# Performance work log

Measured on AMD Instinct MI355X. Metric: run time of the kernel, lower is better.

The kernel has to match this reference:

```python
import jax, jax.numpy as jnp
import numpy as np
import math

EMBED_DIM = 1024
WINDOW = 512


def setup_inputs() -> dict:
    key = jax.random.key(0)
    k_x, k_mb, k_wg, k_bg = jax.random.split(key, 4)
    x = jax.random.normal(k_x, (4, 4096, EMBED_DIM), dtype=jnp.float32)
    memory_bank = jax.random.normal(k_mb, (WINDOW, EMBED_DIM), dtype=jnp.float32)
    # memory_gate: nn.Linear(embed_dim, embed_dim)
    lim = 1.0 / math.sqrt(EMBED_DIM)
    gate_w = jax.random.uniform(k_wg, (EMBED_DIM, EMBED_DIM), jnp.float32, -lim, lim)
    gate_b = jax.random.uniform(k_bg, (EMBED_DIM,), jnp.float32, -lim, lim)
    return {"x": x, "memory_bank": memory_bank, "gate_w": gate_w, "gate_b": gate_b}


def reference(x, memory_bank, gate_w, gate_b):
    d = x.shape[-1]
    # attention scores over fixed memory bank: [B, S, W]
    scores = jnp.einsum("bsd,wd->bsw", x, memory_bank) / jnp.sqrt(jnp.asarray(d, x.dtype))
    attn = jax.nn.softmax(scores, axis=-1)
    retrieved = jnp.einsum("bsw,wd->bsd", attn, memory_bank)
    gate = jax.nn.sigmoid(jnp.einsum("bsd,ed->bse", x, gate_w) + gate_b)
    return gate * x + (1.0 - gate) * retrieved
```

## Files before the change

kernel.cpp:

```cpp
#include <hip/hip_runtime.h>
#include <hip/hip_bf16.h>

#define EMBED 1024
#define WINDOW 512
#define NROWS 16384

typedef __attribute__((ext_vector_type(4))) float f32x4;
typedef __bf16 bf16x8 __attribute__((ext_vector_type(8)));

#define GLDS(g, l)                                                        \
  __builtin_amdgcn_global_load_lds(                                       \
      (const __attribute__((address_space(1))) void*)(const void*)(g),    \
      (__attribute__((address_space(3))) void*)(void*)(l), 16, 0, 0)

__global__ __launch_bounds__(256) void cast_bf16_kernel(
    const float* __restrict__ in, __bf16* __restrict__ out, int n8) {
  int i = blockIdx.x * blockDim.x + threadIdx.x;
  if (i >= n8) return;
  const f32x4* p = (const f32x4*)(in + (size_t)i * 8);
  f32x4 a = p[0], b = p[1];
  bf16x8 o = {(__bf16)a[0], (__bf16)a[1], (__bf16)a[2], (__bf16)a[3],
              (__bf16)b[0], (__bf16)b[1], (__bf16)b[2], (__bf16)b[3]};
  *(bf16x8*)(out + (size_t)i * 8) = o;
}

__global__ __launch_bounds__(256) void transpose_mb_kernel(
    const float* __restrict__ mb, __bf16* __restrict__ mbt) {
  int idx = blockIdx.x * blockDim.x + threadIdx.x;
  int w = idx >> 10, d = idx & 1023;
  mbt[(size_t)d * WINDOW + w] = (__bf16)mb[idx];
}

__global__ __launch_bounds__(256) void softmax_kernel(__bf16* __restrict__ s1) {
  const int row = blockIdx.x * 4 + (threadIdx.x >> 6);
  const int lane = threadIdx.x & 63;
  __bf16* p = s1 + (size_t)row * WINDOW + lane * 8;
  bf16x8 v = *(const bf16x8*)p;
  float f[8];
  float mx = -1e30f;
#pragma unroll
  for (int j = 0; j < 8; ++j) {
    f[j] = (float)v[j] * 0.03125f;
    mx = fmaxf(mx, f[j]);
  }
#pragma unroll
  for (int off = 1; off < 64; off <<= 1) mx = fmaxf(mx, __shfl_xor(mx, off));
  float s = 0.f;
#pragma unroll
  for (int j = 0; j < 8; ++j) {
    f[j] = __expf(f[j] - mx);
    s += f[j];
  }
#pragma unroll
  for (int off = 1; off < 64; off <<= 1) s += __shfl_xor(s, off);
  const float inv = 1.0f / s;
  bf16x8 o;
#pragma unroll
  for (int j = 0; j < 8; ++j) o[j] = (__bf16)(f[j] * inv);
  *(bf16x8*)p = o;
}


#define LOADFRAGS(cb, kk)                                                     \
  {                                                                           \
    const __bf16* As_ = &ldsA[cb][(warp_m * 64 + fr) * 64];                   \
    const __bf16* Bs_ = &ldsB[cb][(warp_n * 64 + fr) * 64];                   \
    const int pg_ = (((kk)*4 + fq) ^ (fr & 7)) * 8;                           \
    _Pragma("unroll") for (int m = 0; m < 4; ++m)                             \
        af[m] = *(const bf16x8*)(As_ + m * 16 * 64 + pg_);                    \
    _Pragma("unroll") for (int n = 0; n < 4; ++n)                             \
        bfv[n] = *(const bf16x8*)(Bs_ + n * 16 * 64 + pg_);                   \
  }

#define MFMA16(ACC)                                                           \
  {                                                                           \
    __builtin_amdgcn_s_barrier();                                             \
    asm volatile("s_waitcnt lgkmcnt(0)" ::: "memory");                        \
    __builtin_amdgcn_s_setprio(1);                                            \
    _Pragma("unroll") for (int m = 0; m < 4; ++m)                             \
        _Pragma("unroll") for (int n = 0; n < 4; ++n)                         \
            ACC[m][n] = __builtin_amdgcn_mfma_f32_16x16x32_bf16(              \
                af[m], bfv[n], ACC[m][n], 0, 0, 0);                           \
    __builtin_amdgcn_s_setprio(0);                                            \
    __builtin_amdgcn_s_barrier();                                             \
  }

#define WAIT6 asm volatile("s_waitcnt vmcnt(6)" ::: "memory")
#define WAIT0 asm volatile("s_waitcnt vmcnt(0)" ::: "memory")

__global__ __launch_bounds__(512, 2) void gemm_scores_kernel(
    const __bf16* __restrict__ xb, const __bf16* __restrict__ mbb,
    __bf16* __restrict__ s1) {
  __shared__ __align__(16) __bf16 ldsA[3][256 * 64];
  __shared__ __align__(16) __bf16 ldsB[3][128 * 64];
  const int tid = threadIdx.x;
  const int lane = tid & 63;
  const int wave = tid >> 6;
  const int bid = blockIdx.x;
  const int xcd = bid & 7;
  const int idx = bid >> 3;
  const int bm = xcd * 8 + (idx & 7);
  const int bn = idx >> 3;
  const int row0 = bm * 256;
  const int col0 = bn * 128;
  const int warp_m = wave >> 1;
  const int warp_n = wave & 1;
  const int srow = lane >> 3;
  const int sgc = (lane & 7) ^ srow;
  const int wv32 = wave * 32;
  const int wv16 = wave * 16;
  const int fr = lane & 15;
  const int fq = lane >> 4;

  const __bf16* aS = xb + (size_t)(row0 + wv32 + srow) * EMBED + sgc * 8;
  const __bf16* bS = mbb + (size_t)(col0 + wv16 + srow) * EMBED + sgc * 8;

#define STAGE_S1(vt, buf)                                                     \
  {                                                                           \
    const int k0_ = (vt)*64;                                                  \
    _Pragma("unroll") for (int c = 0; c < 2; ++c)                             \
        GLDS(aS + (size_t)c * 8 * EMBED + k0_, &ldsA[buf][(wv32 + c * 8) * 64]); \
    GLDS(bS + k0_, &ldsB[buf][wv16 * 64]);                                    \
  }
#define STAGE_S2(vt, buf)                                                     \
  {                                                                           \
    const int k0_ = (vt)*64;                                                  \
    _Pragma("unroll") for (int c = 2; c < 4; ++c)                             \
        GLDS(aS + (size_t)c * 8 * EMBED + k0_, &ldsA[buf][(wv32 + c * 8) * 64]); \
    GLDS(bS + (size_t)8 * EMBED + k0_, &ldsB[buf][(wv16 + 8) * 64]);          \
  }

  f32x4 acc[4][4];
#pragma unroll
  for (int m = 0; m < 4; ++m)
#pragma unroll
    for (int n = 0; n < 4; ++n) acc[m][n] = (f32x4){0.f, 0.f, 0.f, 0.f};
  bf16x8 af[4], bfv[4];

  STAGE_S1(0, 0); STAGE_S2(0, 0);
  STAGE_S1(1, 1); STAGE_S2(1, 1);
  WAIT6;
  __builtin_amdgcn_s_barrier();

  const int NT = 16;
  for (int vt = 0; vt < NT; ++vt) {
    const int cb = vt % 3;
    const int nb = (vt + 2) % 3;
    LOADFRAGS(cb, 0);
    if (vt + 2 < NT) STAGE_S1(vt + 2, nb);
    MFMA16(acc);
    LOADFRAGS(cb, 1);
    if (vt + 2 < NT) STAGE_S2(vt + 2, nb);
    if (vt < NT - 2) { WAIT6; } else if (vt == NT - 2) { WAIT0; }
    MFMA16(acc);
  }
#undef STAGE_S1
#undef STAGE_S2

#pragma unroll
  for (int n = 0; n < 4; ++n) {
    const int col = col0 + warp_n * 64 + n * 16 + fr;
#pragma unroll
    for (int m = 0; m < 4; ++m)
#pragma unroll
      for (int j = 0; j < 4; ++j) {
        const int row = row0 + warp_m * 64 + m * 16 + fq * 4 + j;
        s1[(size_t)row * WINDOW + col] = (__bf16)acc[m][n][j];
      }
  }
}

__global__ __launch_bounds__(512, 2) void dual_fused_kernel(
    const __bf16* __restrict__ s1, const __bf16* __restrict__ xb,
    const __bf16* __restrict__ mbt, const __bf16* __restrict__ gwb,
    const float* __restrict__ gb, float* __restrict__ out) {
  __shared__ __align__(16) __bf16 ldsA[3][256 * 64];
  __shared__ __align__(16) __bf16 ldsB[3][128 * 64];
  const int tid = threadIdx.x;
  const int lane = tid & 63;
  const int wave = tid >> 6;
  const int bid = blockIdx.x;
  const int xcd = bid & 7;
  const int idx = bid >> 3;
  const int bm = xcd * 8 + (idx & 7);
  const int bn = idx >> 3;
  const int row0 = bm * 256;
  const int col0 = bn * 128;
  const int warp_m = wave >> 1;
  const int warp_n = wave & 1;
  const int srow = lane >> 3;
  const int sgc = (lane & 7) ^ srow;
  const int wv32 = wave * 32;
  const int wv16 = wave * 16;
  const int fr = lane & 15;
  const int fq = lane >> 4;

  const __bf16* aR = s1 + (size_t)(row0 + wv32 + srow) * WINDOW + sgc * 8;
  const __bf16* bR = mbt + (size_t)(col0 + wv16 + srow) * WINDOW + sgc * 8;
  const __bf16* aG = xb + (size_t)(row0 + wv32 + srow) * EMBED + sgc * 8;
  const __bf16* bG = gwb + (size_t)(col0 + wv16 + srow) * EMBED + sgc * 8;

#define STAGE_D1(vt, buf)                                                     \
  {                                                                           \
    if ((vt) < 8) {                                                           \
      const int k0_ = (vt)*64;                                                \
      _Pragma("unroll") for (int c = 0; c < 2; ++c)                           \
          GLDS(aR + (size_t)c * 8 * WINDOW + k0_,                             \
               &ldsA[buf][(wv32 + c * 8) * 64]);                              \
      GLDS(bR + k0_, &ldsB[buf][wv16 * 64]);                                  \
    } else {                                                                  \
      const int k0_ = ((vt)-8) * 64;                                          \
      _Pragma("unroll") for (int c = 0; c < 2; ++c)                           \
          GLDS(aG + (size_t)c * 8 * EMBED + k0_,                              \
               &ldsA[buf][(wv32 + c * 8) * 64]);                              \
      GLDS(bG + k0_, &ldsB[buf][wv16 * 64]);                                  \
    }                                                                         \
  }
#define STAGE_D2(vt, buf)                                                     \
  {                                                                           \
    if ((vt) < 8) {                                                           \
      const int k0_ = (vt)*64;                                                \
      _Pragma("unroll") for (int c = 2; c < 4; ++c)                           \
          GLDS(aR + (size_t)c * 8 * WINDOW + k0_,                             \
               &ldsA[buf][(wv32 + c * 8) * 64]);                              \
      GLDS(bR + (size_t)8 * WINDOW + k0_, &ldsB[buf][(wv16 + 8) * 64]);       \
    } else {                                                                  \
      const int k0_ = ((vt)-8) * 64;                                          \
      _Pragma("unroll") for (int c = 2; c < 4; ++c)                           \
          GLDS(aG + (size_t)c * 8 * EMBED + k0_,                              \
               &ldsA[buf][(wv32 + c * 8) * 64]);                              \
      GLDS(bG + (size_t)8 * EMBED + k0_, &ldsB[buf][(wv16 + 8) * 64]);        \
    }                                                                         \
  }

  f32x4 accr[4][4], accg[4][4];
#pragma unroll
  for (int m = 0; m < 4; ++m)
#pragma unroll
    for (int n = 0; n < 4; ++n) {
      accr[m][n] = (f32x4){0.f, 0.f, 0.f, 0.f};
      accg[m][n] = (f32x4){0.f, 0.f, 0.f, 0.f};
    }
  bf16x8 af[4], bfv[4];

  STAGE_D1(0, 0); STAGE_D2(0, 0);
  STAGE_D1(1, 1); STAGE_D2(1, 1);
  WAIT6;
  __builtin_amdgcn_s_barrier();

  const int NT = 24;
  for (int vt = 0; vt < 8; ++vt) {
    const int cb = vt % 3;
    const int nb = (vt + 2) % 3;
    LOADFRAGS(cb, 0);
    STAGE_D1(vt + 2, nb);
    MFMA16(accr);
    LOADFRAGS(cb, 1);
    STAGE_D2(vt + 2, nb);
    WAIT6;
    MFMA16(accr);
  }
  for (int vt = 8; vt < NT; ++vt) {
    const int cb = vt % 3;
    const int nb = (vt + 2) % 3;
    LOADFRAGS(cb, 0);
    if (vt + 2 < NT) STAGE_D1(vt + 2, nb);
    MFMA16(accg);
    LOADFRAGS(cb, 1);
    if (vt + 2 < NT) STAGE_D2(vt + 2, nb);
    if (vt < NT - 2) { WAIT6; } else if (vt == NT - 2) { WAIT0; }
    MFMA16(accg);
  }
#undef STAGE_D1
#undef STAGE_D2

#pragma unroll
  for (int n = 0; n < 4; ++n) {
    const int col = col0 + warp_n * 64 + n * 16 + fr;
    const float bias = gb[col];
#pragma unroll
    for (int m = 0; m < 4; ++m) {
#pragma unroll
      for (int j = 0; j < 4; ++j) {
        const int row = row0 + warp_m * 64 + m * 16 + fq * 4 + j;
        const size_t o = (size_t)row * EMBED + col;
        const float g = 1.0f / (1.0f + __expf(-(accg[m][n][j] + bias)));
        const float xv = (float)xb[o];
        out[o] = g * xv + (1.0f - g) * accr[m][n][j];
      }
    }
  }
}

extern "C" void kernel_launch(void* const* d_in, const int* in_sizes, int n_in,
                              void* d_out, int out_size, void* d_ws,
                              size_t ws_size, hipStream_t stream) {
  const float* x = (const float*)d_in[0];
  const float* mb = (const float*)d_in[1];
  const float* gw = (const float*)d_in[2];
  const float* gb = (const float*)d_in[3];
  float* out = (float*)d_out;

  char* ws = (char*)d_ws;
  __bf16* xb = (__bf16*)(ws);
  __bf16* mbb = (__bf16*)(ws + 33554432);
  __bf16* mbt = (__bf16*)(ws + 34603008);
  __bf16* gwb = (__bf16*)(ws + 35651584);
  __bf16* s1 = (__bf16*)(ws + 37748736);

  cast_bf16_kernel<<<8192, 256, 0, stream>>>(x, xb, 2097152);
  cast_bf16_kernel<<<256, 256, 0, stream>>>(mb, mbb, 65536);
  cast_bf16_kernel<<<512, 256, 0, stream>>>(gw, gwb, 131072);
  transpose_mb_kernel<<<2048, 256, 0, stream>>>(mb, mbt);
  gemm_scores_kernel<<<256, 512, 0, stream>>>(xb, mbb, s1);
  softmax_kernel<<<4096, 256, 0, stream>>>(s1);
  dual_fused_kernel<<<512, 512, 0, stream>>>(s1, xb, mbt, gwb, gb, out);
}
```

Before: 125.5 us.

## Split dual fused GEMM into two 256x256-tile GEMMs with intermediate buffer

```diff
diff --git a/kernel.cpp b/kernel.cpp
--- a/kernel.cpp
+++ b/kernel.cpp
@@ -60,8 +60,7 @@
   *(bf16x8*)p = o;
 }
 
-
-#define LOADFRAGS(cb, kk)                                                     \
+#define SLOADFRAGS(cb, kk)                                                    \
   {                                                                           \
     const __bf16* As_ = &ldsA[cb][(warp_m * 64 + fr) * 64];                   \
     const __bf16* Bs_ = &ldsB[cb][(warp_n * 64 + fr) * 64];                   \
@@ -72,7 +71,7 @@
         bfv[n] = *(const bf16x8*)(Bs_ + n * 16 * 64 + pg_);                   \
   }
 
-#define MFMA16(ACC)                                                           \
+#define SMFMA16(ACC)                                                          \
   {                                                                           \
     __builtin_amdgcn_s_barrier();                                             \
     asm volatile("s_waitcnt lgkmcnt(0)" ::: "memory");                        \
@@ -84,9 +83,6 @@
     __builtin_amdgcn_s_setprio(0);                                            \
     __builtin_amdgcn_s_barrier();                                             \
   }
-
-#define WAIT6 asm volatile("s_waitcnt vmcnt(6)" ::: "memory")
-#define WAIT0 asm volatile("s_waitcnt vmcnt(0)" ::: "memory")
 
 __global__ __launch_bounds__(512, 2) void gemm_scores_kernel(
     const __bf16* __restrict__ xb, const __bf16* __restrict__ mbb,
@@ -139,20 +135,24 @@
 
   STAGE_S1(0, 0); STAGE_S2(0, 0);
   STAGE_S1(1, 1); STAGE_S2(1, 1);
-  WAIT6;
+  asm volatile("s_waitcnt vmcnt(6)" ::: "memory");
   __builtin_amdgcn_s_barrier();
 
   const int NT = 16;
   for (int vt = 0; vt < NT; ++vt) {
     const int cb = vt % 3;
     const int nb = (vt + 2) % 3;
-    LOADFRAGS(cb, 0);
+    SLOADFRAGS(cb, 0);
     if (vt + 2 < NT) STAGE_S1(vt + 2, nb);
-    MFMA16(acc);
-    LOADFRAGS(cb, 1);
+    SMFMA16(acc);
+    SLOADFRAGS(cb, 1);
     if (vt + 2 < NT) STAGE_S2(vt + 2, nb);
-    if (vt < NT - 2) { WAIT6; } else if (vt == NT - 2) { WAIT0; }
-    MFMA16(acc);
+    if (vt < NT - 2) {
+      asm volatile("s_waitcnt vmcnt(6)" ::: "memory");
+    } else if (vt == NT - 2) {
+      asm volatile("s_waitcnt vmcnt(0)" ::: "memory");
+    }
+    SMFMA16(acc);
   }
 #undef STAGE_S1
 #undef STAGE_S2
@@ -170,123 +170,117 @@
   }
 }
 
-__global__ __launch_bounds__(512, 2) void dual_fused_kernel(
-    const __bf16* __restrict__ s1, const __bf16* __restrict__ xb,
-    const __bf16* __restrict__ mbt, const __bf16* __restrict__ gwb,
-    const float* __restrict__ gb, float* __restrict__ out) {
-  __shared__ __align__(16) __bf16 ldsA[3][256 * 64];
-  __shared__ __align__(16) __bf16 ldsB[3][128 * 64];
-  const int tid = threadIdx.x;
-  const int lane = tid & 63;
-  const int wave = tid >> 6;
+template <int NT, int LDA_, int LDB_, int EPI>
+__global__ __launch_bounds__(512, 2) void gemm_mt_kernel(
+    const __bf16* __restrict__ A, const __bf16* __restrict__ B,
+    const float* __restrict__ gb, __bf16* __restrict__ rbb,
+    float* __restrict__ out) {
+  __shared__ __align__(16) __bf16 ldsA[4][256 * 32];
+  __shared__ __align__(16) __bf16 ldsB[4][256 * 32];
+  const int tid = threadIdx.x, lane = tid & 63, wave = tid >> 6;
   const int bid = blockIdx.x;
-  const int xcd = bid & 7;
-  const int idx = bid >> 3;
-  const int bm = xcd * 8 + (idx & 7);
-  const int bn = idx >> 3;
-  const int row0 = bm * 256;
-  const int col0 = bn * 128;
-  const int warp_m = wave >> 1;
-  const int warp_n = wave & 1;
-  const int srow = lane >> 3;
-  const int sgc = (lane & 7) ^ srow;
-  const int wv32 = wave * 32;
-  const int wv16 = wave * 16;
-  const int fr = lane & 15;
-  const int fq = lane >> 4;
-
-  const __bf16* aR = s1 + (size_t)(row0 + wv32 + srow) * WINDOW + sgc * 8;
-  const __bf16* bR = mbt + (size_t)(col0 + wv16 + srow) * WINDOW + sgc * 8;
-  const __bf16* aG = xb + (size_t)(row0 + wv32 + srow) * EMBED + sgc * 8;
-  const __bf16* bG = gwb + (size_t)(col0 + wv16 + srow) * EMBED + sgc * 8;
-
-#define STAGE_D1(vt, buf)                                                     \
-  {                                                                           \
-    if ((vt) < 8) {                                                           \
-      const int k0_ = (vt)*64;                                                \
-      _Pragma("unroll") for (int c = 0; c < 2; ++c)                           \
-          GLDS(aR + (size_t)c * 8 * WINDOW + k0_,                             \
-               &ldsA[buf][(wv32 + c * 8) * 64]);                              \
-      GLDS(bR + k0_, &ldsB[buf][wv16 * 64]);                                  \
-    } else {                                                                  \
-      const int k0_ = ((vt)-8) * 64;                                          \
-      _Pragma("unroll") for (int c = 0; c < 2; ++c)                           \
-          GLDS(aG + (size_t)c * 8 * EMBED + k0_,                              \
-               &ldsA[buf][(wv32 + c * 8) * 64]);                              \
-      GLDS(bG + k0_, &ldsB[buf][wv16 * 64]);                                  \
-    }                                                                         \
-  }
-#define STAGE_D2(vt, buf)                                                     \
-  {                                                                           \
-    if ((vt) < 8) {                                                           \
-      const int k0_ = (vt)*64;                                                \
-      _Pragma("unroll") for (int c = 2; c < 4; ++c)                           \
-          GLDS(aR + (size_t)c * 8 * WINDOW + k0_,                             \
-               &ldsA[buf][(wv32 + c * 8) * 64]);                              \
-      GLDS(bR + (size_t)8 * WINDOW + k0_, &ldsB[buf][(wv16 + 8) * 64]);       \
-    } else {                                                                  \
-      const int k0_ = ((vt)-8) * 64;                                          \
-      _Pragma("unroll") for (int c = 2; c < 4; ++c)                           \
-          GLDS(aG + (size_t)c * 8 * EMBED + k0_,                              \
-               &ldsA[buf][(wv32 + c * 8) * 64]);                              \
-      GLDS(bG + (size_t)8 * EMBED + k0_, &ldsB[buf][(wv16 + 8) * 64]);        \
-    }                                                                         \
-  }
-
-  f32x4 accr[4][4], accg[4][4];
-#pragma unroll
-  for (int m = 0; m < 4; ++m)
-#pragma unroll
-    for (int n = 0; n < 4; ++n) {
-      accr[m][n] = (f32x4){0.f, 0.f, 0.f, 0.f};
-      accg[m][n] = (f32x4){0.f, 0.f, 0.f, 0.f};
+  const int bm = (bid & 7) * 8 + ((bid >> 3) & 7);
+  const int bn = bid >> 6;
+  const int row0 = bm * 256, col0 = bn * 256;
+  const int warp_m = wave >> 2;
+  const int warp_n = wave & 3;
+  const int fr = lane & 15, fq = lane >> 4;
+
+  const int lrow = lane >> 2;
+  const int lsg = (lane & 3) ^ ((lane >> 3) & 3);
+  const __bf16* aSrc = A + (size_t)(row0 + wave * 32 + lrow) * LDA_ + lsg * 8;
+  const __bf16* bSrc = B + (size_t)(col0 + wave * 32 + lrow) * LDB_ + lsg * 8;
+
+#define STG_A(t, c)                                                           \
+  GLDS(aSrc + (size_t)(c) * 16 * LDA_ + (t) * 32,                             \
+       &ldsA[(t) & 3][(wave * 32 + (c) * 16) * 32])
+#define STG_B(t, c)                                                           \
+  GLDS(bSrc + (size_t)(c) * 16 * LDB_ + (t) * 32,                             \
+       &ldsB[(t) & 3][(wave * 32 + (c) * 16) * 32])
+
+  f32x4 acc[8][4];
+#pragma unroll
+  for (int m = 0; m < 8; ++m)
+#pragma unroll
+    for (int n = 0; n < 4; ++n) acc[m][n] = (f32x4){0.f, 0.f, 0.f, 0.f};
+  bf16x8 af[4], bfv[4];
+  const int gA = (fq ^ ((fr >> 1) & 3)) * 8;
+
+  STG_A(0, 0); STG_A(0, 1); STG_B(0, 0); STG_B(0, 1);
+  STG_A(1, 0); STG_A(1, 1); STG_B(1, 0); STG_B(1, 1);
+  STG_A(2, 0); STG_A(2, 1); STG_B(2, 0); STG_B(2, 1);
+  asm volatile("s_waitcnt vmcnt(8)" ::: "memory");
+  __builtin_amdgcn_s_barrier();
+
+  for (int t = 0; t < NT; ++t) {
+    const int s = t & 3;
+    const __bf16* As = &ldsA[s][(warp_m * 128 + fr) * 32 + gA];
+    const __bf16* Bs = &ldsB[s][(warp_n * 64 + fr) * 32 + gA];
+#pragma unroll
+    for (int m = 0; m < 4; ++m) af[m] = *(const bf16x8*)(As + m * 16 * 32);
+#pragma unroll
+    for (int n = 0; n < 4; ++n) bfv[n] = *(const bf16x8*)(Bs + n * 16 * 32);
+    if (t + 3 < NT) { STG_A(t + 3, 0); STG_A(t + 3, 1); }
+    __builtin_amdgcn_s_barrier();
+    asm volatile("s_waitcnt lgkmcnt(0)" ::: "memory");
+    __builtin_amdgcn_s_setprio(1);
+#pragma unroll
+    for (int m = 0; m < 4; ++m)
+#pragma unroll
+      for (int n = 0; n < 4; ++n)
+        acc[m][n] = __builtin_amdgcn_mfma_f32_16x16x32_bf16(af[m], bfv[n],
+                                                            acc[m][n], 0, 0, 0);
+    __builtin_amdgcn_s_setprio(0);
+    __builtin_amdgcn_s_barrier();
+#pragma unroll
+    for (int m = 0; m < 4; ++m)
+      af[m] = *(const bf16x8*)(As + (64 + m * 16) * 32);
+    if (t + 3 < NT) { STG_B(t + 3, 0); STG_B(t + 3, 1); }
+    if (t + 1 < NT) {
+      if (t + 3 < NT) {
+        asm volatile("s_waitcnt vmcnt(8)" ::: "memory");
+      } else if (t + 2 < NT) {
+        asm volatile("s_waitcnt vmcnt(4)" ::: "memory");
+      } else {
+        asm volatile("s_waitcnt vmcnt(0)" ::: "memory");
+      }
     }
-  bf16x8 af[4], bfv[4];
-
-  STAGE_D1(0, 0); STAGE_D2(0, 0);
-  STAGE_D1(1, 1); STAGE_D2(1, 1);
-  WAIT6;
-  __builtin_amdgcn_s_barrier();
-
-  const int NT = 24;
-  for (int vt = 0; vt < 8; ++vt) {
-    const int cb = vt % 3;
-    const int nb = (vt + 2) % 3;
-    LOADFRAGS(cb, 0);
-    STAGE_D1(vt + 2, nb);
-    MFMA16(accr);
-    LOADFRAGS(cb, 1);
-    STAGE_D2(vt + 2, nb);
-    WAIT6;
-    MFMA16(accr);
-  }
-  for (int vt = 8; vt < NT; ++vt) {
-    const int cb = vt % 3;
-    const int nb = (vt + 2) % 3;
-    LOADFRAGS(cb, 0);
-    if (vt + 2 < NT) STAGE_D1(vt + 2, nb);
-    MFMA16(accg);
-    LOADFRAGS(cb, 1);
-    if (vt + 2 < NT) STAGE_D2(vt + 2, nb);
-    if (vt < NT - 2) { WAIT6; } else if (vt == NT - 2) { WAIT0; }
-    MFMA16(accg);
-  }
-#undef STAGE_D1
-#undef STAGE_D2
+    __builtin_amdgcn_s_barrier();
+    asm volatile("s_waitcnt lgkmcnt(0)" ::: "memory");
+    __builtin_amdgcn_s_setprio(1);
+#pragma unroll
+    for (int m = 0; m < 4; ++m)
+#pragma unroll
+      for (int n = 0; n < 4; ++n)
+        acc[4 + m][n] = __builtin_amdgcn_mfma_f32_16x16x32_bf16(
+            af[m], bfv[n], acc[4 + m][n], 0, 0, 0);
+    __builtin_amdgcn_s_setprio(0);
+    __builtin_amdgcn_s_barrier();
+  }
+#undef STG_A
+#undef STG_B
 
 #pragma unroll
   for (int n = 0; n < 4; ++n) {
     const int col = col0 + warp_n * 64 + n * 16 + fr;
-    const float bias = gb[col];
-#pragma unroll
-    for (int m = 0; m < 4; ++m) {
+    float bias = 0.f;
+    if (EPI == 1 || EPI == 3) bias = gb[col];
+#pragma unroll
+    for (int m = 0; m < 8; ++m) {
 #pragma unroll
       for (int j = 0; j < 4; ++j) {
-        const int row = row0 + warp_m * 64 + m * 16 + fq * 4 + j;
+        const int row = row0 + warp_m * 128 + m * 16 + fq * 4 + j;
         const size_t o = (size_t)row * EMBED + col;
-        const float g = 1.0f / (1.0f + __expf(-(accg[m][n][j] + bias)));
-        const float xv = (float)xb[o];
-        out[o] = g * xv + (1.0f - g) * accr[m][n][j];
+        if (EPI == 0) {
+          rbb[o] = (__bf16)acc[m][n][j];
+        } else if (EPI == 2) {
+          out[o] = acc[m][n][j];
+        } else {
+          const float g = 1.0f / (1.0f + __expf(-(acc[m][n][j] + bias)));
+          const float xv = (float)A[(size_t)row * EMBED + col];
+          const float rv = (EPI == 1) ? (float)rbb[o] : out[o];
+          out[o] = g * xv + (1.0f - g) * rv;
+        }
       }
     }
   }
@@ -307,6 +301,8 @@
   __bf16* mbt = (__bf16*)(ws + 34603008);
   __bf16* gwb = (__bf16*)(ws + 35651584);
   __bf16* s1 = (__bf16*)(ws + 37748736);
+  __bf16* rbb = (__bf16*)(ws + 54525952);
+  const bool ws_big = ws_size >= 88080384ull;
 
   cast_bf16_kernel<<<8192, 256, 0, stream>>>(x, xb, 2097152);
   cast_bf16_kernel<<<256, 256, 0, stream>>>(mb, mbb, 65536);
@@ -314,5 +310,15 @@
   transpose_mb_kernel<<<2048, 256, 0, stream>>>(mb, mbt);
   gemm_scores_kernel<<<256, 512, 0, stream>>>(xb, mbb, s1);
   softmax_kernel<<<4096, 256, 0, stream>>>(s1);
-  dual_fused_kernel<<<512, 512, 0, stream>>>(s1, xb, mbt, gwb, gb, out);
-}
+  if (ws_big) {
+    gemm_mt_kernel<16, WINDOW, WINDOW, 0><<<256, 512, 0, stream>>>(
+        s1, mbt, gb, rbb, out);
+    gemm_mt_kernel<32, EMBED, EMBED, 1><<<256, 512, 0, stream>>>(
+        xb, gwb, gb, rbb, out);
+  } else {
+    gemm_mt_kernel<16, WINDOW, WINDOW, 2><<<256, 512, 0, stream>>>(
+        s1, mbt, gb, nullptr, out);
+    gemm_mt_kernel<32, EMBED, EMBED, 3><<<256, 512, 0, stream>>>(
+        xb, gwb, gb, nullptr, out);
+  }
+}
```

New measurement: 159.5 us. 1.27x slower.

## Shrink dual fused GEMM to 128x128 tiles with double-buffered staging

Applied to the files above, without the earlier changes.

```diff
diff --git a/kernel.cpp b/kernel.cpp
--- a/kernel.cpp
+++ b/kernel.cpp
@@ -60,8 +60,7 @@
   *(bf16x8*)p = o;
 }
 
-
-#define LOADFRAGS(cb, kk)                                                     \
+#define SLOADFRAGS(cb, kk)                                                    \
   {                                                                           \
     const __bf16* As_ = &ldsA[cb][(warp_m * 64 + fr) * 64];                   \
     const __bf16* Bs_ = &ldsB[cb][(warp_n * 64 + fr) * 64];                   \
@@ -72,7 +71,7 @@
         bfv[n] = *(const bf16x8*)(Bs_ + n * 16 * 64 + pg_);                   \
   }
 
-#define MFMA16(ACC)                                                           \
+#define SMFMA16(ACC)                                                          \
   {                                                                           \
     __builtin_amdgcn_s_barrier();                                             \
     asm volatile("s_waitcnt lgkmcnt(0)" ::: "memory");                        \
@@ -84,9 +83,6 @@
     __builtin_amdgcn_s_setprio(0);                                            \
     __builtin_amdgcn_s_barrier();                                             \
   }
-
-#define WAIT6 asm volatile("s_waitcnt vmcnt(6)" ::: "memory")
-#define WAIT0 asm volatile("s_waitcnt vmcnt(0)" ::: "memory")
 
 __global__ __launch_bounds__(512, 2) void gemm_scores_kernel(
     const __bf16* __restrict__ xb, const __bf16* __restrict__ mbb,
@@ -139,20 +135,24 @@
 
   STAGE_S1(0, 0); STAGE_S2(0, 0);
   STAGE_S1(1, 1); STAGE_S2(1, 1);
-  WAIT6;
+  asm volatile("s_waitcnt vmcnt(6)" ::: "memory");
   __builtin_amdgcn_s_barrier();
 
   const int NT = 16;
   for (int vt = 0; vt < NT; ++vt) {
     const int cb = vt % 3;
     const int nb = (vt + 2) % 3;
-    LOADFRAGS(cb, 0);
+    SLOADFRAGS(cb, 0);
     if (vt + 2 < NT) STAGE_S1(vt + 2, nb);
-    MFMA16(acc);
-    LOADFRAGS(cb, 1);
+    SMFMA16(acc);
+    SLOADFRAGS(cb, 1);
     if (vt + 2 < NT) STAGE_S2(vt + 2, nb);
-    if (vt < NT - 2) { WAIT6; } else if (vt == NT - 2) { WAIT0; }
-    MFMA16(acc);
+    if (vt < NT - 2) {
+      asm volatile("s_waitcnt vmcnt(6)" ::: "memory");
+    } else if (vt == NT - 2) {
+      asm volatile("s_waitcnt vmcnt(0)" ::: "memory");
+    }
+    SMFMA16(acc);
   }
 #undef STAGE_S1
 #undef STAGE_S2
@@ -170,66 +170,75 @@
   }
 }
 
-__global__ __launch_bounds__(512, 2) void dual_fused_kernel(
+__global__ __launch_bounds__(256, 2) void dual_fused128_kernel(
     const __bf16* __restrict__ s1, const __bf16* __restrict__ xb,
     const __bf16* __restrict__ mbt, const __bf16* __restrict__ gwb,
     const float* __restrict__ gb, float* __restrict__ out) {
-  __shared__ __align__(16) __bf16 ldsA[3][256 * 64];
-  __shared__ __align__(16) __bf16 ldsB[3][128 * 64];
-  const int tid = threadIdx.x;
-  const int lane = tid & 63;
-  const int wave = tid >> 6;
+  __shared__ __align__(16) __bf16 ldsA[2][128 * 64];
+  __shared__ __align__(16) __bf16 ldsB[2][128 * 64];
+  const int tid = threadIdx.x, lane = tid & 63, wave = tid >> 6;
   const int bid = blockIdx.x;
   const int xcd = bid & 7;
-  const int idx = bid >> 3;
-  const int bm = xcd * 8 + (idx & 7);
-  const int bn = idx >> 3;
-  const int row0 = bm * 256;
-  const int col0 = bn * 128;
-  const int warp_m = wave >> 1;
-  const int warp_n = wave & 1;
+  const int g = bid >> 3;
+  const int bm = xcd * 16 + (g & 15);
+  const int bn = g >> 4;
+  const int row0 = bm * 128, col0 = bn * 128;
+  const int warp_m = wave >> 1, warp_n = wave & 1;
+  const int fr = lane & 15, fq = lane >> 4;
   const int srow = lane >> 3;
   const int sgc = (lane & 7) ^ srow;
   const int wv32 = wave * 32;
-  const int wv16 = wave * 16;
-  const int fr = lane & 15;
-  const int fq = lane >> 4;
 
   const __bf16* aR = s1 + (size_t)(row0 + wv32 + srow) * WINDOW + sgc * 8;
-  const __bf16* bR = mbt + (size_t)(col0 + wv16 + srow) * WINDOW + sgc * 8;
+  const __bf16* bR = mbt + (size_t)(col0 + wv32 + srow) * WINDOW + sgc * 8;
   const __bf16* aG = xb + (size_t)(row0 + wv32 + srow) * EMBED + sgc * 8;
-  const __bf16* bG = gwb + (size_t)(col0 + wv16 + srow) * EMBED + sgc * 8;
-
-#define STAGE_D1(vt, buf)                                                     \
+  const __bf16* bG = gwb + (size_t)(col0 + wv32 + srow) * EMBED + sgc * 8;
+
+#define STG(vt, buf)                                                          \
   {                                                                           \
     if ((vt) < 8) {                                                           \
       const int k0_ = (vt)*64;                                                \
-      _Pragma("unroll") for (int c = 0; c < 2; ++c)                           \
+      _Pragma("unroll") for (int c = 0; c < 4; ++c)                           \
           GLDS(aR + (size_t)c * 8 * WINDOW + k0_,                             \
                &ldsA[buf][(wv32 + c * 8) * 64]);                              \
-      GLDS(bR + k0_, &ldsB[buf][wv16 * 64]);                                  \
+      _Pragma("unroll") for (int c = 0; c < 4; ++c)                           \
+          GLDS(bR + (size_t)c * 8 * WINDOW + k0_,                             \
+               &ldsB[buf][(wv32 + c * 8) * 64]);                              \
     } else {                                                                  \
       const int k0_ = ((vt)-8) * 64;                                          \
-      _Pragma("unroll") for (int c = 0; c < 2; ++c)                           \
+      _Pragma("unroll") for (int c = 0; c < 4; ++c)                           \
           GLDS(aG + (size_t)c * 8 * EMBED + k0_,                              \
                &ldsA[buf][(wv32 + c * 8) * 64]);                              \
-      GLDS(bG + k0_, &ldsB[buf][wv16 * 64]);                                  \
+      _Pragma("unroll") for (int c = 0; c < 4; ++c)                           \
+          GLDS(bG + (size_t)c * 8 * EMBED + k0_,                              \
+               &ldsB[buf][(wv32 + c * 8) * 64]);                              \
     }                                                                         \
   }
-#define STAGE_D2(vt, buf)                                                     \
-  {                                                                           \
-    if ((vt) < 8) {                                                           \
-      const int k0_ = (vt)*64;                                                \
-      _Pragma("unroll") for (int c = 2; c < 4; ++c)                           \
-          GLDS(aR + (size_t)c * 8 * WINDOW + k0_,                             \
-               &ldsA[buf][(wv32 + c * 8) * 64]);                              \
-      GLDS(bR + (size_t)8 * WINDOW + k0_, &ldsB[buf][(wv16 + 8) * 64]);       \
-    } else {                                                                  \
-      const int k0_ = ((vt)-8) * 64;                                          \
-      _Pragma("unroll") for (int c = 2; c < 4; ++c)                           \
-          GLDS(aG + (size_t)c * 8 * EMBED + k0_,                              \
-               &ldsA[buf][(wv32 + c * 8) * 64]);                              \
-      GLDS(bG + (size_t)8 * EMBED + k0_, &ldsB[buf][(wv16 + 8) * 64]);        \
+
+#define BARF                                                                  \
+  {                                                                           \
+    asm volatile("" ::: "memory");                                            \
+    __builtin_amdgcn_s_barrier();                                             \
+    asm volatile("" ::: "memory");                                            \
+  }
+
+#define COMPUTE(ACC, cur)                                                     \
+  {                                                                           \
+    const __bf16* As_ = &ldsA[cur][(warp_m * 64 + fr) * 64];                  \
+    const __bf16* Bs_ = &ldsB[cur][(warp_n * 64 + fr) * 64];                  \
+    _Pragma("unroll") for (int kk = 0; kk < 2; ++kk) {                        \
+      const int pg_ = ((kk * 4 + fq) ^ (fr & 7)) * 8;                         \
+      bf16x8 af[4], bfv[4];                                                   \
+      _Pragma("unroll") for (int m = 0; m < 4; ++m)                           \
+          af[m] = *(const bf16x8*)(As_ + m * 16 * 64 + pg_);                  \
+      _Pragma("unroll") for (int n = 0; n < 4; ++n)                           \
+          bfv[n] = *(const bf16x8*)(Bs_ + n * 16 * 64 + pg_);                 \
+      __builtin_amdgcn_s_setprio(1);                                          \
+      _Pragma("unroll") for (int m = 0; m < 4; ++m)                           \
+          _Pragma("unroll") for (int n = 0; n < 4; ++n)                       \
+              ACC[m][n] = __builtin_amdgcn_mfma_f32_16x16x32_bf16(            \
+                  af[m], bfv[n], ACC[m][n], 0, 0, 0);                         \
+      __builtin_amdgcn_s_setprio(0);                                          \
     }                                                                         \
   }
 
@@ -241,38 +250,31 @@
       accr[m][n] = (f32x4){0.f, 0.f, 0.f, 0.f};
       accg[m][n] = (f32x4){0.f, 0.f, 0.f, 0.f};
     }
-  bf16x8 af[4], bfv[4];
-
-  STAGE_D1(0, 0); STAGE_D2(0, 0);
-  STAGE_D1(1, 1); STAGE_D2(1, 1);
-  WAIT6;
-  __builtin_amdgcn_s_barrier();
-
-  const int NT = 24;
+
+  STG(0, 0);
   for (int vt = 0; vt < 8; ++vt) {
-    const int cb = vt % 3;
-    const int nb = (vt + 2) % 3;
-    LOADFRAGS(cb, 0);
-    STAGE_D1(vt + 2, nb);
-    MFMA16(accr);
-    LOADFRAGS(cb, 1);
-    STAGE_D2(vt + 2, nb);
-    WAIT6;
-    MFMA16(accr);
-  }
-  for (int vt = 8; vt < NT; ++vt) {
-    const int cb = vt % 3;
-    const int nb = (vt + 2) % 3;
-    LOADFRAGS(cb, 0);
-    if (vt + 2 < NT) STAGE_D1(vt + 2, nb);
-    MFMA16(accg);
-    LOADFRAGS(cb, 1);
-    if (vt + 2 < NT) STAGE_D2(vt + 2, nb);
-    if (vt < NT - 2) { WAIT6; } else if (vt == NT - 2) { WAIT0; }
-    MFMA16(accg);
-  }
-#undef STAGE_D1
-#undef STAGE_D2
+    const int cur = vt & 1;
+    STG(vt + 1, cur ^ 1);
+    asm volatile("s_waitcnt vmcnt(8)" ::: "memory");
+    BARF;
+    COMPUTE(accr, cur);
+    BARF;
+  }
+  for (int vt = 8; vt < 24; ++vt) {
+    const int cur = vt & 1;
+    if (vt + 1 < 24) {
+      STG(vt + 1, cur ^ 1);
+      asm volatile("s_waitcnt vmcnt(8)" ::: "memory");
+    } else {
+      asm volatile("s_waitcnt vmcnt(0)" ::: "memory");
+    }
+    BARF;
+    COMPUTE(accg, cur);
+    BARF;
+  }
+#undef STG
+#undef COMPUTE
+#undef BARF
 
 #pragma unroll
   for (int n = 0; n < 4; ++n) {
@@ -284,9 +286,9 @@
       for (int j = 0; j < 4; ++j) {
         const int row = row0 + warp_m * 64 + m * 16 + fq * 4 + j;
         const size_t o = (size_t)row * EMBED + col;
-        const float g = 1.0f / (1.0f + __expf(-(accg[m][n][j] + bias)));
+        const float gt = 1.0f / (1.0f + __expf(-(accg[m][n][j] + bias)));
         const float xv = (float)xb[o];
-        out[o] = g * xv + (1.0f - g) * accr[m][n][j];
+        out[o] = gt * xv + (1.0f - gt) * accr[m][n][j];
       }
     }
   }
@@ -314,5 +316,5 @@
   transpose_mb_kernel<<<2048, 256, 0, stream>>>(mb, mbt);
   gemm_scores_kernel<<<256, 512, 0, stream>>>(xb, mbb, s1);
   softmax_kernel<<<4096, 256, 0, stream>>>(s1);
-  dual_fused_kernel<<<512, 512, 0, stream>>>(s1, xb, mbt, gwb, gb, out);
-}
+  dual_fused128_kernel<<<1024, 256, 0, stream>>>(s1, xb, mbt, gwb, gb, out);
+}
```

Result: no change. 124.4 us (-0.9%).
